# Performance work log

Hardware: AMD Instinct MI355X
Metric: run time of the kernel (lower is better)

Reference implementation:

```python
import jax, jax.numpy as jnp
import numpy as np

BATCH = 131072
N = 64          # total bits
PARTS = 16      # len(partition) == dpp_size
M = 4           # bits per part
D = PARTS
EPS = 1e-8


def _colnorm(a):
    return a / jnp.linalg.norm(a, axis=0, keepdims=True)


def setup_inputs() -> dict:
    key = jax.random.key(0)
    k0, k1, k2, k3, k4 = jax.random.split(key, 5)
    x = jax.random.randint(k0, (BATCH, N), 0, 2, dtype=jnp.int32)
    W = jax.random.normal(k1, (PARTS, (1 << M) - 1), dtype=jnp.float32)
    A = _colnorm(jax.random.normal(k2, (D, D), dtype=jnp.float32))
    B = _colnorm(jax.random.normal(k3, (D, D), dtype=jnp.float32))
    C = _colnorm(jax.random.normal(k4, (D, D), dtype=jnp.float32))
    return {"x": x, "W": W, "A": A, "B": B, "C": C}


def reference(x, W, A, B, C):
    batch = x.shape[0]
    # --- Simple PCs (vectorized over the 16 parts): bit-pack each 4-bit part ---
    bits = x.reshape(batch, PARTS, M)                       # contiguous partition
    pow2 = (1 << jnp.arange(M)).astype(jnp.int32)           # [M]
    idx = jnp.sum(bits * pow2, axis=-1)                     # [B, P] in [0, 2^M)
    w = jax.nn.softmax(W, axis=-1)                          # [P, 2^M - 1]
    w = jnp.concatenate([jnp.zeros((PARTS, 1), w.dtype), w], axis=-1)  # [P, 2^M]
    p = w[jnp.arange(PARTS)[None, :], idx]                  # [B, P]

    # --- L matrix: sym PD part + skew part ---
    I = jnp.eye(D, dtype=A.dtype)
    L0 = A.T @ A + (B @ C.T - C @ B.T) + EPS * I            # [D, D]

    # column-scale by p, then force diagonal to 1 where p == 0
    Lp = L0[None, :, :] * p[:, None, :]                     # [B, D, D]
    eye_b = jnp.eye(D, dtype=bool)
    mask = eye_b[None, :, :] & (p == 0.0)[:, :, None]
    Lp = jnp.where(mask, jnp.asarray(1.0, Lp.dtype), Lp)

    sign, logabs = jnp.linalg.slogdet(Lp)                   # [B]
    y = logabs + jnp.log(jax.lax.stop_gradient(sign))       # nan if det < 0 (matches torch.logdet)
    s0, la0 = jnp.linalg.slogdet(L0 + I)
    alpha = la0 + jnp.log(jax.lax.stop_gradient(s0))
    return y - alpha
```

## Files before the change

kernel.cpp:

```cpp
#include <hip/hip_runtime.h>
#include <math.h>

#define BATCH 131072
#define EPS 1e-8f


__global__ void prep_kernel(const float* W, const float* A, const float* Bm,
                            const float* Cm, float* ws) {
    int t = threadIdx.x;
    int i = t >> 4, j = t & 15;
    float s = 0.f;
    #pragma unroll
    for (int k = 0; k < 16; ++k) {
        s += A[k * 16 + i] * A[k * 16 + j];
        s += Bm[i * 16 + k] * Cm[j * 16 + k]
           - Cm[i * 16 + k] * Bm[j * 16 + k];
    }
    if (i == j) s += EPS;
    ws[t] = s;

    if (t < 16) {
        float row[15];
        float mx = -1e30f;
        #pragma unroll
        for (int q = 0; q < 15; ++q) { row[q] = W[t * 15 + q]; mx = fmaxf(mx, row[q]); }
        float se = 0.f;
        #pragma unroll
        for (int q = 0; q < 15; ++q) se += expf(row[q] - mx);
        float lse = mx + logf(se);
        ws[256 + t * 16 + 0] = 0.f;
        #pragma unroll
        for (int q = 0; q < 15; ++q) ws[256 + t * 16 + 1 + q] = row[q] - lse;
    }
}

__global__ __launch_bounds__(64, 1) void table_kernel(const float* ws, float* T,
                                                      float* alphaOut) {
    __shared__ float sL0[256];
    int lt = threadIdx.x;
    #pragma unroll
    for (int q = 0; q < 4; ++q) sL0[lt * 4 + q] = ws[lt * 4 + q];
    __syncthreads();

    unsigned tid = blockIdx.x * 64u + (unsigned)lt;
    if (tid > 65536u) return;
    bool isAlpha = (tid == 65536u);
    unsigned m = isAlpha ? 0xFFFFu : tid;

    float a[16][16];
    #pragma unroll
    for (int i = 0; i < 16; ++i) {
        bool ai = (m >> i) & 1u;
        #pragma unroll
        for (int j = 0; j < 16; ++j) {
            bool aj = (m >> j) & 1u;
            float v = (ai && aj) ? sL0[i * 16 + j] : ((i == j) ? 1.f : 0.f);
            if (isAlpha && i == j) v += 1.f;
            a[i][j] = v;
        }
    }

    float logdet = 0.f;
    #pragma unroll
    for (int k = 0; k < 16; ++k) {
        float piv = a[k][k];
        logdet += __logf(fabsf(piv));
        float inv = 1.0f / piv;
        #pragma unroll
        for (int i2 = k + 1; i2 < 16; ++i2) {
            float f = a[i2][k] * inv;
            #pragma unroll
            for (int j2 = k + 1; j2 < 16; ++j2)
                a[i2][j2] = fmaf(-f, a[k][j2], a[i2][j2]);
        }
    }

    if (isAlpha) *alphaOut = logdet;
    else         T[tid]    = logdet;
}

__global__ __launch_bounds__(256) void main_kernel(const int4* __restrict__ x,
                                                   const float* __restrict__ ws,
                                                   float* __restrict__ out) {
    __shared__ float slw[256];
    int lt = threadIdx.x;
    slw[lt] = ws[256 + lt];
    __syncthreads();

    int b = blockIdx.x * 256 + lt;
    const int4* xb = x + (size_t)b * 16;

    float lw = 0.f;
    unsigned mask = 0;
    #pragma unroll
    for (int j = 0; j < 16; ++j) {
        int4 v = xb[j];
        int idx = v.x + 2 * v.y + 4 * v.z + 8 * v.w;
        lw += slw[j * 16 + idx];
        mask |= (idx != 0 ? 1u : 0u) << j;
    }
    float alpha = ws[512];
    out[b] = lw + ws[1024 + mask] - alpha;
}

extern "C" void kernel_launch(void* const* d_in, const int* in_sizes, int n_in,
                              void* d_out, int out_size, void* d_ws, size_t ws_size,
                              hipStream_t stream) {
    const float* W = (const float*)d_in[1];
    const float* A = (const float*)d_in[2];
    const float* B = (const float*)d_in[3];
    const float* C = (const float*)d_in[4];
    const int4*  x = (const int4*)d_in[0];
    float* ws  = (float*)d_ws;
    float* out = (float*)d_out;

    prep_kernel<<<1, 256, 0, stream>>>(W, A, B, C, ws);
    table_kernel<<<1025, 64, 0, stream>>>(ws, ws + 1024, ws + 512);
    main_kernel<<<BATCH / 256, 256, 0, stream>>>(x, ws, out);
}
```

Measured before the change: 95.30 us.

## Replace 65536-entry logdet table with complement-minor formula via inverse of L0

Removes the table kernel that factored all 65536 masked 16x16 matrices. Instead it inverts L0 once in the prep kernel and uses the identity det(L_S) = det(L0) * det(inv(L0)[Z,Z]), where Z is the set of zero parts, solving a small minor of at most 5x5 per sample. Samples with more zeros are pushed to an overflow list for a cleanup kernel that does a full 16x16 factorization. The main kernel now uses 16 threads per sample with ballot and shuffle reductions. The cleanup is capped at a fixed overflow size, so samples beyond it would get wrong results, and the inverse-based path may lose numerical accuracy.

```diff
diff --git a/kernel.cpp b/kernel.cpp
--- a/kernel.cpp
+++ b/kernel.cpp
@@ -3,12 +3,18 @@
 
 #define BATCH 131072
 #define EPS 1e-8f
-
-
-__global__ void prep_kernel(const float* W, const float* A, const float* Bm,
-                            const float* Cm, float* ws) {
+#define OVF_CAP 16384u
+
+
+__global__ __launch_bounds__(256) void prep_kernel(
+    const float* __restrict__ W, const float* __restrict__ A,
+    const float* __restrict__ Bm, const float* __restrict__ Cm,
+    float* __restrict__ ws) {
+    __shared__ float sAug[16 * 34];
+    __shared__ float sLI[16 * 17];
     int t = threadIdx.x;
     int i = t >> 4, j = t & 15;
+
     float s = 0.f;
     #pragma unroll
     for (int k = 0; k < 16; ++k) {
@@ -17,7 +23,36 @@
            - Cm[i * 16 + k] * Bm[j * 16 + k];
     }
     if (i == j) s += EPS;
-    ws[t] = s;
+    sAug[i * 34 + j] = s;
+    sAug[i * 34 + 16 + j] = (i == j) ? 1.f : 0.f;
+    sLI[i * 17 + j] = s + ((i == j) ? 1.f : 0.f);
+    __syncthreads();
+
+    float logdetAcc = 0.f, alphaAcc = 0.f;
+    for (int k = 0; k < 16; ++k) {
+        float piv  = sAug[k * 34 + k];
+        float f    = sAug[i * 34 + k];
+        float pivL = sLI[k * 17 + k];
+        float g    = sLI[i * 17 + k];
+        logdetAcc += __logf(fabsf(piv));
+        alphaAcc  += __logf(fabsf(pivL));
+        __syncthreads();
+        if (t < 32) sAug[k * 34 + t] *= 1.f / piv;
+        __syncthreads();
+        if (i != k) {
+            sAug[i * 34 + j]      = fmaf(-f, sAug[k * 34 + j],      sAug[i * 34 + j]);
+            sAug[i * 34 + 16 + j] = fmaf(-f, sAug[k * 34 + 16 + j], sAug[i * 34 + 16 + j]);
+        }
+        if (i > k) {
+            sLI[i * 17 + j] = fmaf(-g / pivL, sLI[k * 17 + j], sLI[i * 17 + j]);
+        }
+        __syncthreads();
+    }
+
+    ws[272 + i * 16 + j] = sAug[i * 34 + 16 + j];
+    if (t == 0) { ws[528] = logdetAcc; ws[529] = alphaAcc; }
+    if (t == 17) ((unsigned*)ws)[530] = 0u;
+    if (t == 18) ws[271] = 0.f;
 
     if (t < 16) {
         float row[15];
@@ -28,93 +63,141 @@
         #pragma unroll
         for (int q = 0; q < 15; ++q) se += expf(row[q] - mx);
         float lse = mx + logf(se);
-        ws[256 + t * 16 + 0] = 0.f;
-        #pragma unroll
-        for (int q = 0; q < 15; ++q) ws[256 + t * 16 + 1 + q] = row[q] - lse;
-    }
-}
-
-__global__ __launch_bounds__(64, 1) void table_kernel(const float* ws, float* T,
-                                                      float* alphaOut) {
-    __shared__ float sL0[256];
+        ws[t * 17 + 0] = 0.f;
+        #pragma unroll
+        for (int q = 0; q < 15; ++q) ws[t * 17 + 1 + q] = row[q] - lse;
+    }
+}
+
+__global__ __launch_bounds__(256) void main_kernel(const int4* __restrict__ x4,
+                                                   float* __restrict__ ws,
+                                                   float* __restrict__ out) {
+    __shared__ float sLW[272];
+    __shared__ float sM[272];
+    int t = threadIdx.x;
+    sLW[t] = ws[t];
+    if (t < 16) sLW[256 + t] = ws[256 + t];
+    sM[(t >> 4) * 17 + (t & 15)] = ws[272 + t];
+    __syncthreads();
+
+    int l = t & 15;
+    int grp = t >> 4;
+    int b = blockIdx.x * 16 + grp;
+
+    int4 v = x4[(size_t)blockIdx.x * 256 + t];
+    int idx = v.x + 2 * v.y + 4 * v.z + 8 * v.w;
+    float lw = sLW[l * 17 + idx];
+
+    unsigned lane = t & 63;
+    unsigned long long wmask = __ballot(idx != 0);
+    unsigned gm = (unsigned)((wmask >> (lane & 48)) & 0xFFFFull);
+
+    lw += __shfl_xor(lw, 1);
+    lw += __shfl_xor(lw, 2);
+    lw += __shfl_xor(lw, 4);
+    lw += __shfl_xor(lw, 8);
+
+    if (l == 0) {
+        unsigned zb = (~gm) & 0xFFFFu;
+        int z = __popc(zb);
+        float base = lw + ws[528] - ws[529];
+        if (z <= 5) {
+            int zi[5];
+            unsigned tt = zb;
+            #pragma unroll
+            for (int q = 0; q < 5; ++q) {
+                zi[q] = tt ? (__ffs(tt) - 1) : 0;
+                tt &= tt - 1;
+            }
+            float m[5][5];
+            #pragma unroll
+            for (int r = 0; r < 5; ++r)
+                #pragma unroll
+                for (int c = 0; c < 5; ++c)
+                    m[r][c] = (r < z && c < z) ? sM[zi[r] * 17 + zi[c]]
+                                               : ((r == c) ? 1.f : 0.f);
+            float logd = 0.f;
+            #pragma unroll
+            for (int k = 0; k < 5; ++k) {
+                float piv = m[k][k];
+                logd += __logf(fabsf(piv));
+                float inv = 1.0f / piv;
+                #pragma unroll
+                for (int r = k + 1; r < 5; ++r) {
+                    float f = m[r][k] * inv;
+                    #pragma unroll
+                    for (int c = k + 1; c < 5; ++c)
+                        m[r][c] = fmaf(-f, m[k][c], m[r][c]);
+                }
+            }
+            out[b] = base + logd;
+        } else {
+            unsigned pos = atomicAdd(((unsigned*)ws) + 530, 1u);
+            if (pos < OVF_CAP) {
+                ((int*)ws)[544 + 2 * pos] = b;
+                ((int*)ws)[545 + 2 * pos] = (int)zb;
+            }
+            out[b] = base;
+        }
+    }
+}
+
+__global__ __launch_bounds__(64, 1) void cleanup_kernel(const float* __restrict__ ws,
+                                                        float* __restrict__ out) {
+    __shared__ float sM[256];
     int lt = threadIdx.x;
     #pragma unroll
-    for (int q = 0; q < 4; ++q) sL0[lt * 4 + q] = ws[lt * 4 + q];
+    for (int q = 0; q < 4; ++q) sM[lt * 4 + q] = ws[272 + lt * 4 + q];
     __syncthreads();
 
-    unsigned tid = blockIdx.x * 64u + (unsigned)lt;
-    if (tid > 65536u) return;
-    bool isAlpha = (tid == 65536u);
-    unsigned m = isAlpha ? 0xFFFFu : tid;
-
-    float a[16][16];
-    #pragma unroll
-    for (int i = 0; i < 16; ++i) {
-        bool ai = (m >> i) & 1u;
+    unsigned n = ((const unsigned*)ws)[530];
+    if (n > OVF_CAP) n = OVF_CAP;
+    unsigned stride = 8u * 64u;
+    for (unsigned ii = blockIdx.x * 64u + (unsigned)lt; ii < n; ii += stride) {
+        int b = ((const int*)ws)[544 + 2 * ii];
+        unsigned Z = (unsigned)((const int*)ws)[545 + 2 * ii];
+
+        float a[16][16];
         #pragma unroll
         for (int j = 0; j < 16; ++j) {
-            bool aj = (m >> j) & 1u;
-            float v = (ai && aj) ? sL0[i * 16 + j] : ((i == j) ? 1.f : 0.f);
-            if (isAlpha && i == j) v += 1.f;
-            a[i][j] = v;
-        }
-    }
-
-    float logdet = 0.f;
-    #pragma unroll
-    for (int k = 0; k < 16; ++k) {
-        float piv = a[k][k];
-        logdet += __logf(fabsf(piv));
-        float inv = 1.0f / piv;
-        #pragma unroll
-        for (int i2 = k + 1; i2 < 16; ++i2) {
-            float f = a[i2][k] * inv;
-            #pragma unroll
-            for (int j2 = k + 1; j2 < 16; ++j2)
-                a[i2][j2] = fmaf(-f, a[k][j2], a[i2][j2]);
-        }
-    }
-
-    if (isAlpha) *alphaOut = logdet;
-    else         T[tid]    = logdet;
-}
-
-__global__ __launch_bounds__(256) void main_kernel(const int4* __restrict__ x,
-                                                   const float* __restrict__ ws,
-                                                   float* __restrict__ out) {
-    __shared__ float slw[256];
-    int lt = threadIdx.x;
-    slw[lt] = ws[256 + lt];
-    __syncthreads();
-
-    int b = blockIdx.x * 256 + lt;
-    const int4* xb = x + (size_t)b * 16;
-
-    float lw = 0.f;
-    unsigned mask = 0;
-    #pragma unroll
-    for (int j = 0; j < 16; ++j) {
-        int4 v = xb[j];
-        int idx = v.x + 2 * v.y + 4 * v.z + 8 * v.w;
-        lw += slw[j * 16 + idx];
-        mask |= (idx != 0 ? 1u : 0u) << j;
-    }
-    float alpha = ws[512];
-    out[b] = lw + ws[1024 + mask] - alpha;
+            bool on = (Z >> j) & 1u;
+            #pragma unroll
+            for (int i = 0; i < 16; ++i) {
+                float v2 = on ? sM[i * 16 + j] : 0.f;
+                if (i == j && !on) v2 = 1.f;
+                a[i][j] = v2;
+            }
+        }
+        float logdet = 0.f;
+        #pragma unroll
+        for (int k = 0; k < 16; ++k) {
+            float piv = a[k][k];
+            logdet += __logf(fabsf(piv));
+            float inv = 1.0f / piv;
+            #pragma unroll
+            for (int i2 = k + 1; i2 < 16; ++i2) {
+                float f = a[i2][k] * inv;
+                #pragma unroll
+                for (int j2 = k + 1; j2 < 16; ++j2)
+                    a[i2][j2] = fmaf(-f, a[k][j2], a[i2][j2]);
+            }
+        }
+        out[b] += logdet;
+    }
 }
 
 extern "C" void kernel_launch(void* const* d_in, const int* in_sizes, int n_in,
                               void* d_out, int out_size, void* d_ws, size_t ws_size,
                               hipStream_t stream) {
+    const int4*  x = (const int4*)d_in[0];
     const float* W = (const float*)d_in[1];
     const float* A = (const float*)d_in[2];
     const float* B = (const float*)d_in[3];
     const float* C = (const float*)d_in[4];
-    const int4*  x = (const int4*)d_in[0];
     float* ws  = (float*)d_ws;
     float* out = (float*)d_out;
 
     prep_kernel<<<1, 256, 0, stream>>>(W, A, B, C, ws);
-    table_kernel<<<1025, 64, 0, stream>>>(ws, ws + 1024, ws + 512);
-    main_kernel<<<BATCH / 256, 256, 0, stream>>>(x, ws, out);
-}
+    main_kernel<<<BATCH / 16, 256, 0, stream>>>(x, ws, out);
+    cleanup_kernel<<<8, 64, 0, stream>>>(ws, out);
+}
```

Result: slower. 105.7 us (+10.9%).
